# Kernel optimization log

Measured on AMD Instinct MI355X. Metric: run time of the kernel, lower is better.

Reference implementation:

```python
import jax, jax.numpy as jnp
import numpy as np

EPS = 1e-5

def batchnorm2d(x, gamma, beta):
    # training-mode BN over (N, T, V) per channel; x: [N, C, T, V]
    mean = jnp.mean(x, axis=(0, 2, 3), keepdims=True)
    var = jnp.var(x, axis=(0, 2, 3), keepdims=True)
    xhat = (x - mean) * jax.lax.rsqrt(var + EPS)
    return xhat * gamma[None, :, None, None] + beta[None, :, None, None]

def temporal_shift(x, theta, stride):
    # learnable per-channel temporal shift with linear interpolation, zero pad
    # x: [N, C, T, V], theta: [C]
    N, C, T, V = x.shape
    T_out = T // stride
    t = jnp.arange(T_out, dtype=theta.dtype)
    pos = t[None, :] * stride + theta[:, None]          # [C, T_out]
    i0 = jnp.floor(pos).astype(jnp.int32)
    frac = (pos - i0.astype(theta.dtype))[None, :, :, None]  # [1,C,T_out,1]
    cidx = jnp.arange(C)[:, None]                        # [C, 1]

    def gather(idx):
        valid = (idx >= 0) & (idx < T)
        g = x[:, cidx, jnp.clip(idx, 0, T - 1), :]       # [N, C, T_out, V]
        return jnp.where(valid[None, :, :, None], g, 0.0)

    return gather(i0) * (1.0 - frac) + gather(i0 + 1) * frac

def setup_inputs() -> dict:
    key = jax.random.key(0)
    k = jax.random.split(key, 6)
    N, Cin, Cout, T, V = 64, 256, 256, 64, 25
    x = jax.random.normal(k[0], (N, Cin, T, V), dtype=jnp.float32)
    # kaiming normal fan_out for 1x1 conv: std = sqrt(2 / (Cout*1*1))
    conv_w = jax.random.normal(k[1], (Cout, Cin), dtype=jnp.float32) * np.float32(np.sqrt(2.0 / Cout))
    conv_b = jnp.zeros((Cout,), dtype=jnp.float32)
    bn1_g = jnp.ones((Cin,), dtype=jnp.float32)
    bn1_b = jnp.zeros((Cin,), dtype=jnp.float32)
    bn2_g = jnp.ones((Cin,), dtype=jnp.float32)   # bn_init(bn2, 1)
    bn2_b = jnp.zeros((Cin,), dtype=jnp.float32)
    theta_in = jax.random.uniform(k[2], (Cin,), jnp.float32, -1.0, 1.0)
    theta_out = jax.random.uniform(k[3], (Cout,), jnp.float32, -1.0, 1.0)
    return {"x": x, "conv_w": conv_w, "conv_b": conv_b,
            "bn1_g": bn1_g, "bn1_b": bn1_b, "bn2_g": bn2_g, "bn2_b": bn2_b,
            "theta_in": theta_in, "theta_out": theta_out}

def reference(x, conv_w, conv_b, bn1_g, bn1_b, bn2_g, bn2_b, theta_in, theta_out):
    stride = 1
    h = batchnorm2d(x, bn1_g, bn1_b)
    h = temporal_shift(h, theta_in, 1)
    h = jnp.einsum('nctv,oc->notv', h, conv_w) + conv_b[None, :, None, None]
    h = jax.nn.relu(h)
    h = temporal_shift(h, theta_out, stride)
    h = batchnorm2d(h, bn2_g, bn2_b)
    return h
```

## Files before the change

kernel.cpp:

```cpp
#include <hip/hip_runtime.h>


#define EPSV 1e-5f
constexpr int Nn = 64, Cc = 256, Tt = 64, Vv = 25;
constexpr int TV = Tt * Vv;
constexpr int CTV = Cc * TV;
constexpr float Minv = 1.0f / (Nn * TV);

typedef short short8 __attribute__((ext_vector_type(8)));
typedef float floatx4 __attribute__((ext_vector_type(4)));

__device__ __forceinline__ unsigned short f2bf(float f) {
    unsigned int u = __builtin_bit_cast(unsigned int, f);
    u += 0x7FFFu + ((u >> 16) & 1u);
    return (unsigned short)(u >> 16);
}
__device__ __forceinline__ float bf2f(unsigned short h) {
    unsigned int u = ((unsigned int)h) << 16;
    return __builtin_bit_cast(float, u);
}

__global__ __launch_bounds__(256) void k_wconv(const float* __restrict__ w,
                                               unsigned short* __restrict__ wb) {
    int i = blockIdx.x * 256 + threadIdx.x;
    wb[i] = f2bf(w[i]);
}

__global__ __launch_bounds__(256) void k_bn1_stats(const float* __restrict__ x,
                                                   float* __restrict__ sacc,
                                                   float* __restrict__ qacc) {
    int c = blockIdx.y, ng = blockIdx.x, tid = threadIdx.x;
    const float* xp = x + (size_t)(ng * 8) * CTV + (size_t)c * TV;
    float s = 0.f, q = 0.f;
    for (int n = 0; n < 8; ++n) {
        const float4* p = (const float4*)(xp + (size_t)n * CTV);
        for (int i = tid; i < 400; i += 256) {
            float4 v = p[i];
            s += (v.x + v.y) + (v.z + v.w);
            q += (v.x * v.x + v.y * v.y) + (v.z * v.z + v.w * v.w);
        }
    }
    for (int off = 32; off; off >>= 1) { s += __shfl_down(s, off); q += __shfl_down(q, off); }
    if ((tid & 63) == 0) { atomicAdd(&sacc[c], s); atomicAdd(&qacc[c], q); }
}

__global__ __launch_bounds__(256) void k_bnparams(const float* __restrict__ sacc,
                                                  const float* __restrict__ qacc,
                                                  const float* __restrict__ g,
                                                  const float* __restrict__ b,
                                                  const float* __restrict__ theta,
                                                  float* __restrict__ s1,
                                                  float* __restrict__ t1,
                                                  int* __restrict__ pd,
                                                  float* __restrict__ pf) {
    int c = threadIdx.x;
    float mean = sacc[c] * Minv;
    float var = qacc[c] * Minv - mean * mean;
    float sc = g[c] * rsqrtf(var + EPSV);
    s1[c] = sc;
    t1[c] = b[c] - mean * sc;
    float th = theta[c];
    float fd = floorf(th);
    pd[c] = (int)fd;
    pf[c] = th - fd;
}

__global__ __launch_bounds__(256) void k_bn1_shift(const float* __restrict__ x,
                                                   const float* __restrict__ s1,
                                                   const float* __restrict__ t1,
                                                   const int* __restrict__ pd,
                                                   const float* __restrict__ pf,
                                                   unsigned short* __restrict__ ht) {
    int c0 = blockIdx.x * 16;
    int tile = blockIdx.y;
    int n = blockIdx.z;
    int tid = threadIdx.x;
    __shared__ __attribute__((aligned(16))) float lds[16][460];
    __shared__ float psc[16], ptc[16], pfr[16];
    __shared__ int pdd[16], pww[16];

    if (tid < 16) {
        int c = c0 + tid;
        int d = pd[c];
        pdd[tid] = d;
        pww[tid] = 28 + d * 25;
        pfr[tid] = pf[c];
        psc[tid] = s1[c];
        ptc[tid] = t1[c];
    }

    int E0 = tile * 400;
    int lo = E0 - 28; if (lo < 0) lo = 0;
    int hi = E0 + 428; if (hi > 1600) hi = 1600;
    int ldsoff = lo - (E0 - 28);
    int nf4 = (hi - lo) >> 2;
    {
        int ci = tid >> 4, li = tid & 15;
        const float4* xrow = (const float4*)(x + (size_t)n * CTV + (size_t)(c0 + ci) * TV + lo);
        float* lrow = &lds[ci][ldsoff];
        for (int i = li; i < nf4; i += 16)
            *(float4*)(lrow + i * 4) = xrow[i];
    }
    __syncthreads();

    int oct = tid & 1, tvr = tid >> 1;
    unsigned short* outb = ht + (size_t)n * CTV + c0 + oct * 8;
    for (int tv_l = tvr; tv_l < 400; tv_l += 128) {
        int e = E0 + tv_l;
        int t = e / 25;
        unsigned int wrds[4];
#pragma unroll
        for (int k = 0; k < 8; ++k) {
            int ci = oct * 8 + k;
            int i0 = t + pdd[ci];
            int w0 = tv_l + pww[ci];
            float x0 = lds[ci][w0];
            float x1 = lds[ci][w0 + 25];
            float sc = psc[ci], tc = ptc[ci], f = pfr[ci];
            float b0 = ((unsigned)i0 < 64u) ? (x0 * sc + tc) : 0.f;
            float b1 = ((unsigned)(i0 + 1) < 64u) ? (x1 * sc + tc) : 0.f;
            unsigned short hb = f2bf(b0 + f * (b1 - b0));
            if (k & 1) wrds[k >> 1] |= ((unsigned int)hb) << 16;
            else       wrds[k >> 1] = hb;
        }
        uint4 st = { wrds[0], wrds[1], wrds[2], wrds[3] };
        *(uint4*)(outb + (size_t)e * 256) = st;
    }
}

__global__ __launch_bounds__(256) void k_gemm(const unsigned short* __restrict__ ht,
                                              const unsigned short* __restrict__ wb,
                                              const float* __restrict__ bias,
                                              unsigned short* __restrict__ y) {
    int n = blockIdx.z;
    int o0 = blockIdx.y * 64;
    int tv0 = blockIdx.x * 64;
    int tid = threadIdx.x;
    int wave = tid >> 6, lane = tid & 63;
    int quad = lane >> 4, l16 = lane & 15;
    __shared__ __attribute__((aligned(16))) unsigned short A[64][40];
    __shared__ __attribute__((aligned(16))) unsigned short B[64][40];
    floatx4 acc[4] = {};
    const unsigned short* hb = ht + (size_t)n * CTV;
    int lrow = tid >> 2;
    int lk = (tid & 3) * 8;
    for (int k0 = 0; k0 < 256; k0 += 32) {
        const uint4 av = *(const uint4*)(wb + (size_t)(o0 + lrow) * 256 + k0 + lk);
        const uint4 bv = *(const uint4*)(hb + (size_t)(tv0 + lrow) * 256 + k0 + lk);
        __syncthreads();
        *(uint4*)&A[lrow][lk] = av;
        *(uint4*)&B[lrow][lk] = bv;
        __syncthreads();
        short8 af = *(const short8*)&A[wave * 16 + l16][quad * 8];
#pragma unroll
        for (int jt = 0; jt < 4; ++jt) {
            short8 bf = *(const short8*)&B[jt * 16 + l16][quad * 8];
            acc[jt] = __builtin_amdgcn_mfma_f32_16x16x32_bf16(af, bf, acc[jt], 0, 0, 0);
        }
    }
    unsigned short* yb = y + (size_t)n * CTV;
#pragma unroll
    for (int jt = 0; jt < 4; ++jt) {
#pragma unroll
        for (int r = 0; r < 4; ++r) {
            int o = o0 + wave * 16 + quad * 4 + r;
            int tv = tv0 + jt * 16 + l16;
            float vv = acc[jt][r] + bias[o];
            vv = vv > 0.f ? vv : 0.f;
            yb[(size_t)o * TV + tv] = f2bf(vv);
        }
    }
}

__global__ __launch_bounds__(256) void k_bn2_stats(const unsigned short* __restrict__ y,
                                                   const float* __restrict__ theta,
                                                   float* __restrict__ sacc,
                                                   float* __restrict__ qacc) {
    int o = blockIdx.y, ng = blockIdx.x, tid = threadIdx.x;
    __shared__ __attribute__((aligned(16))) unsigned short row[1600];
    float th = theta[o];
    float fd = floorf(th);
    int d = (int)fd;
    float f = th - fd;
    float s = 0.f, q = 0.f;
    for (int n = ng * 8; n < ng * 8 + 8; ++n) {
        const uint4* yp = (const uint4*)(y + (size_t)n * CTV + (size_t)o * TV);
        __syncthreads();
        if (tid < 200) ((uint4*)row)[tid] = yp[tid];
        __syncthreads();
        for (int e = tid; e < 1600; e += 256) {
            int t = e / 25, v = e - t * 25;
            int i0 = t + d, i1 = i0 + 1;
            float a0 = ((unsigned)i0 < 64u) ? bf2f(row[i0 * 25 + v]) : 0.f;
            float a1 = ((unsigned)i1 < 64u) ? bf2f(row[i1 * 25 + v]) : 0.f;
            float z = (1.f - f) * a0 + f * a1;
            s += z; q += z * z;
        }
    }
    for (int off = 32; off; off >>= 1) { s += __shfl_down(s, off); q += __shfl_down(q, off); }
    if ((tid & 63) == 0) { atomicAdd(&sacc[o], s); atomicAdd(&qacc[o], q); }
}

__global__ __launch_bounds__(256) void k_bn2_apply(const unsigned short* __restrict__ y,
                                                   const float* __restrict__ theta,
                                                   const float* __restrict__ sacc,
                                                   const float* __restrict__ qacc,
                                                   const float* __restrict__ g,
                                                   const float* __restrict__ b,
                                                   float* __restrict__ out) {
    int o = blockIdx.y, n = blockIdx.x, tid = threadIdx.x;
    __shared__ __attribute__((aligned(16))) unsigned short row[1600];
    float th = theta[o];
    float fd = floorf(th);
    int d = (int)fd;
    float f = th - fd;
    float mean = sacc[o] * Minv;
    float var = qacc[o] * Minv - mean * mean;
    float sc = g[o] * rsqrtf(var + EPSV);
    float tc = b[o] - mean * sc;
    const uint4* yp = (const uint4*)(y + (size_t)n * CTV + (size_t)o * TV);
    if (tid < 200) ((uint4*)row)[tid] = yp[tid];
    __syncthreads();
    float4* op = (float4*)(out + (size_t)n * CTV + (size_t)o * TV);
    for (int i = tid; i < 400; i += 256) {
        float4 r;
        int e = i * 4;
#pragma unroll
        for (int k = 0; k < 4; ++k) {
            int ee = e + k;
            int t = ee / 25, v = ee - t * 25;
            int i0 = t + d, i1 = i0 + 1;
            float a0 = ((unsigned)i0 < 64u) ? bf2f(row[i0 * 25 + v]) : 0.f;
            float a1 = ((unsigned)i1 < 64u) ? bf2f(row[i1 * 25 + v]) : 0.f;
            ((float*)&r)[k] = ((1.f - f) * a0 + f * a1) * sc + tc;
        }
        op[i] = r;
    }
}

extern "C" void kernel_launch(void* const* d_in, const int* in_sizes, int n_in,
                              void* d_out, int out_size, void* d_ws, size_t ws_size,
                              hipStream_t stream) {
    const float* x      = (const float*)d_in[0];
    const float* conv_w = (const float*)d_in[1];
    const float* conv_b = (const float*)d_in[2];
    const float* bn1_g  = (const float*)d_in[3];
    const float* bn1_b  = (const float*)d_in[4];
    const float* bn2_g  = (const float*)d_in[5];
    const float* bn2_b  = (const float*)d_in[6];
    const float* th_in  = (const float*)d_in[7];
    const float* th_out = (const float*)d_in[8];
    float* out = (float*)d_out;

    char* ws = (char*)d_ws;
    unsigned short* ht = (unsigned short*)ws;
    unsigned short* yy = (unsigned short*)(ws + 52428800);
    unsigned short* wb = (unsigned short*)(ws + 104857600);
    float* sacc1 = (float*)(ws + 104988672);
    float* qacc1 = sacc1 + 256;
    float* sacc2 = qacc1 + 256;
    float* qacc2 = sacc2 + 256;
    float* s1    = qacc2 + 256;
    float* t1    = s1 + 256;
    float* pf1   = t1 + 256;
    int*   pd1   = (int*)(pf1 + 256);

    hipMemsetAsync((void*)sacc1, 0, 4 * 256 * sizeof(float), stream);
    hipLaunchKernelGGL(k_wconv, dim3(256), dim3(256), 0, stream, conv_w, wb);
    hipLaunchKernelGGL(k_bn1_stats, dim3(8, 256), dim3(256), 0, stream, x, sacc1, qacc1);
    hipLaunchKernelGGL(k_bnparams, dim3(1), dim3(256), 0, stream,
                       sacc1, qacc1, bn1_g, bn1_b, th_in, s1, t1, pd1, pf1);
    hipLaunchKernelGGL(k_bn1_shift, dim3(16, 4, 64), dim3(256), 0, stream,
                       x, s1, t1, pd1, pf1, ht);
    hipLaunchKernelGGL(k_gemm, dim3(25, 4, 64), dim3(256), 0, stream, ht, wb, conv_b, yy);
    hipLaunchKernelGGL(k_bn2_stats, dim3(8, 256), dim3(256), 0, stream, yy, th_out, sacc2, qacc2);
    hipLaunchKernelGGL(k_bn2_apply, dim3(64, 256), dim3(256), 0, stream,
                       yy, th_out, sacc2, qacc2, bn2_g, bn2_b, out);
}
```

Before: 345.3 us.

## Enlarge GEMM tiles with direct-to-LDS loads and fold small kernels into neighbors

The GEMM now uses 128x128 output tiles across the flattened N*TV dimension, with each wave computing a 4x4 grid of MFMAs. Operands are loaded straight from global memory into LDS with global_load_lds, which gives more reuse per loaded tile and removes the register staging step. Weight conversion is folded into the BN1 stats kernel as an extra row of blocks, and the BN parameter computation is recomputed inside the shift kernel, which removes two launches. The costs are higher register pressure and an unpadded LDS layout that may cause bank conflicts.

```diff
diff --git a/kernel.cpp b/kernel.cpp
--- a/kernel.cpp
+++ b/kernel.cpp
@@ -19,17 +19,23 @@
     unsigned int u = ((unsigned int)h) << 16;
     return __builtin_bit_cast(float, u);
 }
-
-__global__ __launch_bounds__(256) void k_wconv(const float* __restrict__ w,
-                                               unsigned short* __restrict__ wb) {
-    int i = blockIdx.x * 256 + threadIdx.x;
-    wb[i] = f2bf(w[i]);
+__device__ __forceinline__ void gload_lds16(const void* g, void* l) {
+    __builtin_amdgcn_global_load_lds((const __attribute__((address_space(1))) void*)g,
+                                     (__attribute__((address_space(3))) void*)l, 16, 0, 0);
 }
 
 __global__ __launch_bounds__(256) void k_bn1_stats(const float* __restrict__ x,
+                                                   const float* __restrict__ w,
+                                                   unsigned short* __restrict__ wb,
                                                    float* __restrict__ sacc,
                                                    float* __restrict__ qacc) {
     int c = blockIdx.y, ng = blockIdx.x, tid = threadIdx.x;
+    if (c == 256) {
+        int base = ng * 8192 + tid;
+#pragma unroll
+        for (int i = 0; i < 32; ++i) wb[base + i * 256] = f2bf(w[base + i * 256]);
+        return;
+    }
     const float* xp = x + (size_t)(ng * 8) * CTV + (size_t)c * TV;
     float s = 0.f, q = 0.f;
     for (int n = 0; n < 8; ++n) {
@@ -44,32 +50,12 @@
     if ((tid & 63) == 0) { atomicAdd(&sacc[c], s); atomicAdd(&qacc[c], q); }
 }
 
-__global__ __launch_bounds__(256) void k_bnparams(const float* __restrict__ sacc,
-                                                  const float* __restrict__ qacc,
-                                                  const float* __restrict__ g,
-                                                  const float* __restrict__ b,
-                                                  const float* __restrict__ theta,
-                                                  float* __restrict__ s1,
-                                                  float* __restrict__ t1,
-                                                  int* __restrict__ pd,
-                                                  float* __restrict__ pf) {
-    int c = threadIdx.x;
-    float mean = sacc[c] * Minv;
-    float var = qacc[c] * Minv - mean * mean;
-    float sc = g[c] * rsqrtf(var + EPSV);
-    s1[c] = sc;
-    t1[c] = b[c] - mean * sc;
-    float th = theta[c];
-    float fd = floorf(th);
-    pd[c] = (int)fd;
-    pf[c] = th - fd;
-}
-
 __global__ __launch_bounds__(256) void k_bn1_shift(const float* __restrict__ x,
-                                                   const float* __restrict__ s1,
-                                                   const float* __restrict__ t1,
-                                                   const int* __restrict__ pd,
-                                                   const float* __restrict__ pf,
+                                                   const float* __restrict__ sacc,
+                                                   const float* __restrict__ qacc,
+                                                   const float* __restrict__ g,
+                                                   const float* __restrict__ b,
+                                                   const float* __restrict__ theta,
                                                    unsigned short* __restrict__ ht) {
     int c0 = blockIdx.x * 16;
     int tile = blockIdx.y;
@@ -81,12 +67,17 @@
 
     if (tid < 16) {
         int c = c0 + tid;
-        int d = pd[c];
+        float mean = sacc[c] * Minv;
+        float var = qacc[c] * Minv - mean * mean;
+        float sc = g[c] * rsqrtf(var + EPSV);
+        float th = theta[c];
+        float fd = floorf(th);
+        int d = (int)fd;
         pdd[tid] = d;
         pww[tid] = 28 + d * 25;
-        pfr[tid] = pf[c];
-        psc[tid] = s1[c];
-        ptc[tid] = t1[c];
+        pfr[tid] = th - fd;
+        psc[tid] = sc;
+        ptc[tid] = b[c] - mean * sc;
     }
 
     int E0 = tile * 400;
@@ -132,42 +123,57 @@
                                               const unsigned short* __restrict__ wb,
                                               const float* __restrict__ bias,
                                               unsigned short* __restrict__ y) {
-    int n = blockIdx.z;
-    int o0 = blockIdx.y * 64;
-    int tv0 = blockIdx.x * 64;
+    int j0 = blockIdx.x * 128;
+    int o0 = blockIdx.y * 128;
     int tid = threadIdx.x;
-    int wave = tid >> 6, lane = tid & 63;
+    int w = tid >> 6, lane = tid & 63;
     int quad = lane >> 4, l16 = lane & 15;
-    __shared__ __attribute__((aligned(16))) unsigned short A[64][40];
-    __shared__ __attribute__((aligned(16))) unsigned short B[64][40];
-    floatx4 acc[4] = {};
-    const unsigned short* hb = ht + (size_t)n * CTV;
-    int lrow = tid >> 2;
-    int lk = (tid & 3) * 8;
+    __shared__ __attribute__((aligned(16))) unsigned short A[128 * 32];
+    __shared__ __attribute__((aligned(16))) unsigned short B[128 * 32];
+    floatx4 acc[4][4] = {};
+    int srow = w * 32 + (lane >> 2);
+    int skcol = (lane & 3) * 8;
+    const unsigned short* wp0 = wb + (size_t)(o0 + srow) * 256 + skcol;
+    const unsigned short* hp0 = ht + (size_t)(j0 + srow) * 256 + skcol;
+    int oh = w >> 1, jh = w & 1;
     for (int k0 = 0; k0 < 256; k0 += 32) {
-        const uint4 av = *(const uint4*)(wb + (size_t)(o0 + lrow) * 256 + k0 + lk);
-        const uint4 bv = *(const uint4*)(hb + (size_t)(tv0 + lrow) * 256 + k0 + lk);
-        __syncthreads();
-        *(uint4*)&A[lrow][lk] = av;
-        *(uint4*)&B[lrow][lk] = bv;
-        __syncthreads();
-        short8 af = *(const short8*)&A[wave * 16 + l16][quad * 8];
-#pragma unroll
-        for (int jt = 0; jt < 4; ++jt) {
-            short8 bf = *(const short8*)&B[jt * 16 + l16][quad * 8];
-            acc[jt] = __builtin_amdgcn_mfma_f32_16x16x32_bf16(af, bf, acc[jt], 0, 0, 0);
-        }
-    }
-    unsigned short* yb = y + (size_t)n * CTV;
-#pragma unroll
-    for (int jt = 0; jt < 4; ++jt) {
+        __syncthreads();
+#pragma unroll
+        for (int a = 0; a < 2; ++a) {
+            gload_lds16(wp0 + (size_t)a * 16 * 256 + k0, A + (w * 32 + a * 16) * 32);
+            gload_lds16(hp0 + (size_t)a * 16 * 256 + k0, B + (w * 32 + a * 16) * 32);
+        }
+        __syncthreads();
+        short8 af[4], bf[4];
+#pragma unroll
+        for (int m = 0; m < 4; ++m)
+            af[m] = *(const short8*)&A[(oh * 64 + m * 16 + l16) * 32 + quad * 8];
+#pragma unroll
+        for (int jt = 0; jt < 4; ++jt)
+            bf[jt] = *(const short8*)&B[(jh * 64 + jt * 16 + l16) * 32 + quad * 8];
+#pragma unroll
+        for (int m = 0; m < 4; ++m)
+#pragma unroll
+            for (int jt = 0; jt < 4; ++jt)
+                acc[m][jt] = __builtin_amdgcn_mfma_f32_16x16x32_bf16(af[m], bf[jt], acc[m][jt], 0, 0, 0);
+    }
+    int jbase = j0 + jh * 64;
+    int n = jbase / 1600;
+    int tvb = jbase - n * 1600;
+    unsigned short* yb = y + (size_t)n * CTV + tvb;
+#pragma unroll
+    for (int m = 0; m < 4; ++m) {
+        int o = o0 + oh * 64 + m * 16 + quad * 4;
 #pragma unroll
         for (int r = 0; r < 4; ++r) {
-            int o = o0 + wave * 16 + quad * 4 + r;
-            int tv = tv0 + jt * 16 + l16;
-            float vv = acc[jt][r] + bias[o];
-            vv = vv > 0.f ? vv : 0.f;
-            yb[(size_t)o * TV + tv] = f2bf(vv);
+            float bia = bias[o + r];
+            unsigned short* yrow = yb + (size_t)(o + r) * TV;
+#pragma unroll
+            for (int jt = 0; jt < 4; ++jt) {
+                float vv = acc[m][jt][r] + bia;
+                vv = vv > 0.f ? vv : 0.f;
+                yrow[jt * 16 + l16] = f2bf(vv);
+            }
         }
     }
 }
@@ -260,19 +266,13 @@
     float* qacc1 = sacc1 + 256;
     float* sacc2 = qacc1 + 256;
     float* qacc2 = sacc2 + 256;
-    float* s1    = qacc2 + 256;
-    float* t1    = s1 + 256;
-    float* pf1   = t1 + 256;
-    int*   pd1   = (int*)(pf1 + 256);
 
     hipMemsetAsync((void*)sacc1, 0, 4 * 256 * sizeof(float), stream);
-    hipLaunchKernelGGL(k_wconv, dim3(256), dim3(256), 0, stream, conv_w, wb);
-    hipLaunchKernelGGL(k_bn1_stats, dim3(8, 256), dim3(256), 0, stream, x, sacc1, qacc1);
-    hipLaunchKernelGGL(k_bnparams, dim3(1), dim3(256), 0, stream,
-                       sacc1, qacc1, bn1_g, bn1_b, th_in, s1, t1, pd1, pf1);
+    hipLaunchKernelGGL(k_bn1_stats, dim3(8, 257), dim3(256), 0, stream,
+                       x, conv_w, wb, sacc1, qacc1);
     hipLaunchKernelGGL(k_bn1_shift, dim3(16, 4, 64), dim3(256), 0, stream,
-                       x, s1, t1, pd1, pf1, ht);
-    hipLaunchKernelGGL(k_gemm, dim3(25, 4, 64), dim3(256), 0, stream, ht, wb, conv_b, yy);
+                       x, sacc1, qacc1, bn1_g, bn1_b, th_in, ht);
+    hipLaunchKernelGGL(k_gemm, dim3(800, 2), dim3(256), 0, stream, ht, wb, conv_b, yy);
     hipLaunchKernelGGL(k_bn2_stats, dim3(8, 256), dim3(256), 0, stream, yy, th_out, sacc2, qacc2);
     hipLaunchKernelGGL(k_bn2_apply, dim3(64, 256), dim3(256), 0, stream,
                        yy, th_out, sacc2, qacc2, bn2_g, bn2_b, out);
```

Result: faster. 332.2 us (-3.8%).
